# Optimization experiments

Measured on AMD Instinct MI355X. Metric: run time of the kernel, lower is better.

The kernel has to match this reference:

```python
import jax, jax.numpy as jnp
import numpy as np

B, N, D_IN, D_OUT, NHOP = 16, 1024, 128, 128, 3


def setup_inputs() -> dict:
    key = jax.random.key(0)
    ks = jax.random.split(key, 7)
    x = jax.random.normal(ks[0], (B, N, D_IN), dtype=jnp.float32)
    # sparse-ish binary adjacency (float, as in the torch model) with self loops
    adj = (jax.random.uniform(ks[1], (B, N, N)) < 0.05).astype(jnp.float32)
    adj = jnp.maximum(adj, jnp.eye(N, dtype=jnp.float32)[None])
    # learned params (torch nn.Linear default-ish init scale)
    s_in = 1.0 / np.sqrt(D_IN)
    s_out = 1.0 / np.sqrt(2 * D_OUT)
    W_w = jax.random.uniform(ks[2], (D_OUT, D_IN), minval=-s_in, maxval=s_in, dtype=jnp.float32)
    W_b = jax.random.uniform(ks[3], (D_OUT,), minval=-s_in, maxval=s_in, dtype=jnp.float32)
    A = jax.random.normal(ks[4], (D_OUT, D_OUT), dtype=jnp.float32) * 0.02  # nn.Parameter(zeros) would kill signal; use small init
    gate_w = jax.random.uniform(ks[5], (1, 2 * D_OUT), minval=-s_out, maxval=s_out, dtype=jnp.float32)
    gate_b = jax.random.uniform(ks[6], (1,), minval=-s_out, maxval=s_out, dtype=jnp.float32)
    return {"x": x, "adj": adj, "W_w": W_w, "W_b": W_b, "A": A,
            "gate_w": gate_w, "gate_b": gate_b}


def reference(x, adj, W_w, W_b, A, gate_w, gate_b):
    # h = W(x): [B,N,D_OUT]
    h = jnp.einsum('bnd,od->bno', x, W_w) + W_b
    # bilinear score e[b,j,k] = (h A)_j . h_k, symmetrized
    e = jnp.einsum('bjl,bkl->bjk', jnp.einsum('bjd,de->bje', h, A), h)
    e = e + jnp.swapaxes(e, 1, 2)
    # masked softmax over dim=1 (as in the torch code), then re-mask
    att = jnp.where(adj > 0, e, jnp.zeros((), dtype=e.dtype))
    att = jax.nn.softmax(att, axis=1)
    att = att * adj
    retval = h
    for _ in range(NHOP):
        az = jax.nn.relu(jnp.einsum('bij,bjk->bik', att, retval))
        gate_in = jnp.concatenate([h, az], axis=-1)            # [B,N,2*D_OUT]
        coeff = jax.nn.sigmoid(jnp.einsum('bnf,of->bno', gate_in, gate_w) + gate_b)  # [B,N,1]
        retval = coeff * h + (1.0 - coeff) * az
    return retval
```

## Files before the change

### kernel.cpp

```cpp
#include <hip/hip_runtime.h>
#include <math.h>

#define Bn 16
#define Nn 1024
#define Dn 128

typedef unsigned short ushort;
typedef unsigned long long u64;
typedef short short8 __attribute__((ext_vector_type(8)));
typedef float f32x4 __attribute__((ext_vector_type(4)));
typedef ushort us8 __attribute__((ext_vector_type(8)));
typedef ushort us4 __attribute__((ext_vector_type(4)));

__device__ __forceinline__ ushort f2bf(float f) {
    unsigned u = __float_as_uint(f);
    u += 0x7fff + ((u >> 16) & 1);
    return (ushort)(u >> 16);
}
__device__ __forceinline__ float bf2f(ushort s) {
    return __uint_as_float(((unsigned)s) << 16);
}

#if defined(__has_builtin)
#if __has_builtin(__builtin_amdgcn_global_load_lds)
#define HAVE_GLL 1
#endif
#endif
#ifndef HAVE_GLL
#define HAVE_GLL 0
#endif

typedef __attribute__((address_space(1))) void as1_t;
typedef __attribute__((address_space(3))) void as3_t;

__device__ __forceinline__ void stage_group(const void* gbase, void* lbase, int lane) {
#if HAVE_GLL
    __builtin_amdgcn_global_load_lds((as1_t*)((const char*)gbase + lane * 16),
                                     (as3_t*)lbase, 16, 0, 0);
#else
    *(us8*)((char*)lbase + lane * 16) = *(const us8*)((const char*)gbase + lane * 16);
#endif
}


__global__ __launch_bounds__(256) void k_ph0(const float* __restrict__ Ww,
                                             const float* __restrict__ A,
                                             const float* __restrict__ adj,
                                             ushort* __restrict__ Whi, ushort* __restrict__ Wlo,
                                             ushort* __restrict__ Shi, ushort* __restrict__ Slo,
                                             float* __restrict__ Z, u64* __restrict__ bm) {
    int L = blockIdx.x, t = threadIdx.x;
    if (L < 64) {
        int i = L * 256 + t;
        float w = Ww[i];
        ushort wh = f2bf(w);
        Whi[i] = wh;
        Wlo[i] = f2bf(w - bf2f(wh));
        int e = i >> 7, d = i & 127;
        float s = A[i] + A[d * Dn + e];
        ushort sh = f2bf(s);
        Shi[i] = sh;
        Slo[i] = f2bf(s - bf2f(sh));
        Z[i] = (float)Nn;
    }
    int gwv = L * 4 + (t >> 6);
    int lane = t & 63;
    #pragma unroll 4
    for (int it = 0; it < 16; ++it) {
        int pair = gwv * 16 + it;
        const float* p = adj + (size_t)pair * 256 + lane * 4;
        float4 v = *(const float4*)p;
        u64 b0 = __ballot(v.x > 0.f);
        u64 b1 = __ballot(v.y > 0.f);
        u64 b2 = __ballot(v.z > 0.f);
        u64 b3 = __ballot(v.w > 0.f);
        if (lane == 0) {
            u64* d = bm + (size_t)pair * 4;
            d[0] = b0; d[1] = b1; d[2] = b2; d[3] = b3;
        }
    }
}

__global__ __launch_bounds__(256) void k_h(const float* __restrict__ x,
                                           const float* __restrict__ Wb,
                                           const ushort* __restrict__ Whi,
                                           const ushort* __restrict__ Wlo,
                                           const ushort* __restrict__ Shi,
                                           const ushort* __restrict__ Slo,
                                           float* __restrict__ h,
                                           ushort* __restrict__ h16f,
                                           ushort* __restrict__ g16f) {
    int I0 = blockIdx.x * 16;
    int t = threadIdx.x, w = t >> 6, lane = t & 63;
    int m = lane & 15, q = lane >> 4;

    __shared__ float xs[16][Dn + 4];
    __shared__ float hs[16][Dn + 4];
    __shared__ float gs_[16][Dn + 4];

    {
        int r = t >> 4, c8 = (t & 15) * 8;
        const float* src = x + (size_t)(I0 + r) * Dn + c8;
        *(float4*)&xs[r][c8]     = *(const float4*)(src);
        *(float4*)&xs[r][c8 + 4] = *(const float4*)(src + 4);
    }
    __syncthreads();

    f32x4 acc0 = {0,0,0,0}, acc1 = {0,0,0,0};
    #pragma unroll
    for (int ks = 0; ks < 4; ++ks) {
        int k0 = q * 8 + ks * 32;
        float v[8]; short8 ahi, alo;
        *(float4*)(v)     = *(const float4*)(&xs[m][k0]);
        *(float4*)(v + 4) = *(const float4*)(&xs[m][k0 + 4]);
        #pragma unroll
        for (int j = 0; j < 8; ++j) {
            ushort hi = f2bf(v[j]);
            ahi[j] = (short)hi;
            alo[j] = (short)f2bf(v[j] - bf2f(hi));
        }
        #pragma unroll
        for (int nn = 0; nn < 2; ++nn) {
            int brow = (w * 2 + nn) * 16 + m;
            short8 bhi = __builtin_bit_cast(short8, ((const us8*)(Whi + (size_t)brow * Dn))[q + ks * 4]);
            short8 blo = __builtin_bit_cast(short8, ((const us8*)(Wlo + (size_t)brow * Dn))[q + ks * 4]);
            f32x4 acc = nn ? acc1 : acc0;
            acc = __builtin_amdgcn_mfma_f32_16x16x32_bf16(ahi, bhi, acc, 0, 0, 0);
            acc = __builtin_amdgcn_mfma_f32_16x16x32_bf16(alo, bhi, acc, 0, 0, 0);
            acc = __builtin_amdgcn_mfma_f32_16x16x32_bf16(ahi, blo, acc, 0, 0, 0);
            if (nn) acc1 = acc; else acc0 = acc;
        }
    }
    #pragma unroll
    for (int nn = 0; nn < 2; ++nn) {
        int col = (w * 2 + nn) * 16 + m;
        float bias = Wb[col];
        f32x4 acc = nn ? acc1 : acc0;
        #pragma unroll
        for (int r = 0; r < 4; ++r) {
            int rl = q * 4 + r;
            float hv = acc[r] + bias;
            h[(size_t)(I0 + rl) * Dn + col] = hv;
            hs[rl][col] = hv;
        }
    }
    __syncthreads();

    f32x4 bcc0 = {0,0,0,0}, bcc1 = {0,0,0,0};
    #pragma unroll
    for (int ks = 0; ks < 4; ++ks) {
        int k0 = q * 8 + ks * 32;
        float v[8]; short8 ahi, alo;
        *(float4*)(v)     = *(const float4*)(&hs[m][k0]);
        *(float4*)(v + 4) = *(const float4*)(&hs[m][k0 + 4]);
        #pragma unroll
        for (int j = 0; j < 8; ++j) {
            ushort hi = f2bf(v[j]);
            ahi[j] = (short)hi;
            alo[j] = (short)f2bf(v[j] - bf2f(hi));
        }
        #pragma unroll
        for (int nn = 0; nn < 2; ++nn) {
            int brow = (w * 2 + nn) * 16 + m;
            short8 bhi = __builtin_bit_cast(short8, ((const us8*)(Shi + (size_t)brow * Dn))[q + ks * 4]);
            short8 blo = __builtin_bit_cast(short8, ((const us8*)(Slo + (size_t)brow * Dn))[q + ks * 4]);
            f32x4 acc = nn ? bcc1 : bcc0;
            acc = __builtin_amdgcn_mfma_f32_16x16x32_bf16(ahi, bhi, acc, 0, 0, 0);
            acc = __builtin_amdgcn_mfma_f32_16x16x32_bf16(alo, bhi, acc, 0, 0, 0);
            acc = __builtin_amdgcn_mfma_f32_16x16x32_bf16(ahi, blo, acc, 0, 0, 0);
            if (nn) bcc1 = acc; else bcc0 = acc;
        }
    }
    #pragma unroll
    for (int nn = 0; nn < 2; ++nn) {
        int col = (w * 2 + nn) * 16 + m;
        f32x4 acc = nn ? bcc1 : bcc0;
        #pragma unroll
        for (int r = 0; r < 4; ++r)
            gs_[q * 4 + r][col] = acc[r];
    }
    __syncthreads();

    {
        int kc = t >> 6, mm = (t >> 2) & 15, qq = t & 3;
        int cb = kc * 32 + qq * 8;
        us8 oh, oa;
        #pragma unroll
        for (int e = 0; e < 8; ++e) {
            oh[e] = f2bf(hs[mm][cb + e]);
            oa[e] = f2bf(gs_[mm][cb + e]);
        }
        size_t U = (size_t)(I0 >> 4) * 256 + kc * 64 + qq * 16 + mm;
        ((us8*)h16f)[U] = oh;
        ((us8*)g16f)[U] = oa;
    }
}

__global__ __launch_bounds__(256, 4) void k_scores(const ushort* __restrict__ g16f,
                                                   const ushort* __restrict__ h16f,
                                                   const u64* __restrict__ bm,
                                                   ushort* __restrict__ Ef,
                                                   float* __restrict__ Z) {
    int L = blockIdx.x;
    int b    = ((L & 7) << 1) | (L >> 11);
    int tile = (L >> 3) & 255;
    int I0 = (tile >> 4) << 6;
    int J0 = (tile & 15) << 6;
    int t = threadIdx.x, wid = t >> 6, lane = t & 63;
    int loff = lane * 16;

    __shared__ __align__(16) char smem[18432];
    float (*sc)[68] = (float(*)[68])smem;
    float (*cz)[64] = (float(*)[64])(smem + 17408);

    {
        const char* hbp = (const char*)h16f + (size_t)b * 262144;
        for (int g = wid; g < 16; g += 4) {
            int rt_l = g >> 2, kk = g & 3;
            stage_group(hbp + ((size_t)((J0 >> 4) + rt_l) * 256 + kk * 64) * 16,
                        smem + g * 1024, lane);
        }
    }
    short8 afr[4];
    {
        const char* gbp = (const char*)g16f + (size_t)b * 262144
                        + (size_t)((I0 >> 4) + wid) * 4096 + loff;
        #pragma unroll
        for (int ks = 0; ks < 4; ++ks)
            afr[ks] = __builtin_bit_cast(short8, *(const us8*)(gbp + ks * 1024));
    }
    __syncthreads();

    f32x4 acc[4] = {};
    #pragma unroll
    for (int ks = 0; ks < 4; ++ks) {
        #pragma unroll
        for (int nt = 0; nt < 4; ++nt) {
            short8 bb = __builtin_bit_cast(short8,
                *(const us8*)(smem + (nt * 4 + ks) * 1024 + loff));
            acc[nt] = __builtin_amdgcn_mfma_f32_16x16x32_bf16(afr[ks], bb, acc[nt], 0, 0, 0);
        }
    }
    __syncthreads();

    {
        int m = lane & 15, q = lane >> 4;
        #pragma unroll
        for (int nt = 0; nt < 4; ++nt)
            #pragma unroll
            for (int r = 0; r < 4; ++r)
                sc[wid * 16 + q * 4 + r][nt * 16 + m] = acc[nt][r];
    }
    __syncthreads();

    int row16 = t >> 4, c = t & 15;
    int bitc = ((J0 >> 2) & 63) + c;
    float colsum[4] = {0.f, 0.f, 0.f, 0.f};
    #pragma unroll
    for (int it = 0; it < 4; ++it) {
        int row = it * 16 + row16;
        const u64* wp = bm + ((size_t)(b * Nn + I0 + row) * 4 + (J0 >> 8)) * 4;
        u64 wj[4] = {wp[0], wp[1], wp[2], wp[3]};
        float s4[4];
        *(float4*)s4 = *(const float4*)(&sc[row][c * 4]);
        us4 e4;
        #pragma unroll
        for (int j = 0; j < 4; ++j) {
            float ex = __expf(s4[j]);
            bool on = (wj[j] >> bitc) & 1;
            e4[j] = f2bf(on ? ex : 0.f);
            colsum[j] += on ? (ex - 1.0f) : 0.f;
        }
        size_t base = ((((size_t)b * 64 + (I0 >> 4) + it) * 32 + (J0 >> 5) + (c >> 3)) * 512)
                    + (size_t)((c & 7) >> 1) * 128 + row16 * 8 + (c & 1) * 4;
        *(us4*)(Ef + base) = e4;
    }
    #pragma unroll
    for (int j = 0; j < 4; ++j) {
        colsum[j] += __shfl_xor(colsum[j], 16, 64);
        colsum[j] += __shfl_xor(colsum[j], 32, 64);
    }
    if (lane < 16) {
        #pragma unroll
        for (int j = 0; j < 4; ++j) cz[wid][lane * 4 + j] = colsum[j];
    }
    __syncthreads();
    if (t < 64) {
        float s = cz[0][t] + cz[1][t] + cz[2][t] + cz[3][t];
        atomicAdd(&Z[b * Nn + J0 + t], s);
    }
}

__global__ __launch_bounds__(256) void k_prep(const float* __restrict__ src,
                                              const float* __restrict__ Z,
                                              ushort* __restrict__ Tf) {
    int b = blockIdx.y;
    int j0 = blockIdx.x * 64;
    int t = threadIdx.x;
    __shared__ float ls[64][129];
    __shared__ float iz[64];
    if (t < 64) iz[t] = 1.0f / Z[b * Nn + j0 + t];
    __syncthreads();
    #pragma unroll
    for (int it = 0; it < 8; ++it) {
        int idx = it * 256 + t;
        int j = idx >> 5, k4 = (idx & 31) * 4;
        float4 v = *(const float4*)(src + ((size_t)b * Nn + j0 + j) * Dn + k4);
        float z = iz[j];
        ls[j][k4] = v.x * z; ls[j][k4 + 1] = v.y * z;
        ls[j][k4 + 2] = v.z * z; ls[j][k4 + 3] = v.w * z;
    }
    __syncthreads();
    int k = t & 127, half = t >> 7;
    us8 o[4];
    #pragma unroll
    for (int qq = 0; qq < 4; ++qq) {
        us8 tmp;
        #pragma unroll
        for (int e = 0; e < 8; ++e)
            tmp[e] = f2bf(ls[half * 32 + qq * 8 + e][k]);
        o[qq] = tmp;
    }
    size_t G = (size_t)(k >> 4) * 32 + (j0 >> 5) + half;
    ushort* dst = Tf + (size_t)b * 131072 + G * 512 + (size_t)(k & 15) * 8;
    #pragma unroll
    for (int qq = 0; qq < 4; ++qq)
        *(us8*)(dst + qq * 128) = o[qq];
}

#define SSTAGE(BUF, gc) do {                                                           \
    _Pragma("unroll")                                                                  \
    for (int j = 0; j < 8; ++j) {                                                      \
        int g = rr * 8 + j;                         \
        stage_group(tfb + ((size_t)(g >> 2) * 32 + (gc) * 4 + (g & 3)) * 1024,         \
                    sbase + (BUF) * 32768 + g * 1024, lane);                           \
    }                                                                                  \
} while (0)

#define ELD(SET, gc) do {                                                              \
    _Pragma("unroll")                                                                  \
    for (int kk = 0; kk < 4; ++kk)                                                     \
        SET[kk] = __builtin_bit_cast(short8,                                           \
            *(const us8*)(ebase + ((gc) * 4 + kk) * 1024));                            \
} while (0)

#define SMFMA(BUF, SET) do {                                                           \
    __builtin_amdgcn_s_setprio(1);                                                     \
    _Pragma("unroll")                                                                  \
    for (int kk = 0; kk < 4; ++kk) {                                                   \
        _Pragma("unroll")                                                              \
        for (int nt = 0; nt < 8; ++nt) {                                               \
            short8 bf = __builtin_bit_cast(short8,                                     \
                *(const us8*)(sbase + (BUF) * 32768 + (nt * 4 + kk) * 1024 + loff));   \
            acc[nt] = __builtin_amdgcn_mfma_f32_16x16x32_bf16(SET[kk], bf, acc[nt], 0, 0, 0); \
        }                                                                              \
    }                                                                                  \
    __builtin_amdgcn_s_setprio(0);                                                     \
} while (0)

#define WAITB(NC) do {                                                                 \
    asm volatile("s_waitcnt vmcnt(" #NC ")" ::: "memory");                             \
    __builtin_amdgcn_s_barrier();                                                      \
} while (0)

__global__ __launch_bounds__(512, 1) void k_hop(const ushort* __restrict__ Ef,
                                                const ushort* __restrict__ Tf,
                                                const float* __restrict__ h,
                                                const float* __restrict__ Z,
                                                const float* __restrict__ gw,
                                                const float* __restrict__ gb,
                                                ushort* __restrict__ Tfn,
                                                float* __restrict__ out,
                                                int last) {
    int L = blockIdx.x;
    int b   = ((L & 7) << 1) | (L >> 7);
    int rtp = (L >> 3) & 15;
    int t = threadIdx.x, w = t >> 6, lane = t & 63;
    int m = lane & 15, q = lane >> 4;
    int rr = w & 3, ks = w >> 2;
    int rt = rtp * 4 + rr;
    int I0 = rt << 4;
    int loff = lane * 16;

    __shared__ __align__(16) char smem[131072];
    char* sbase = smem + ks * 65536;

    const char* tfb   = (const char*)Tf + (size_t)b * 262144;
    const char* ebase = (const char*)Ef + (size_t)(b * 64 + rt) * 32768 + loff;

    float hv[8][4], izr[4], gwa[8], gwz[8];
    float gb0 = gb[0];
    size_t hbase = ((size_t)b * Nn + I0) * Dn;
    if (ks == 0) {
        #pragma unroll
        for (int r = 0; r < 4; ++r) izr[r] = 1.0f / Z[b * Nn + I0 + q * 4 + r];
        #pragma unroll
        for (int nt = 0; nt < 8; ++nt) {
            gwa[nt] = gw[nt * 16 + m];
            gwz[nt] = gw[Dn + nt * 16 + m];
            #pragma unroll
            for (int r = 0; r < 4; ++r)
                hv[nt][r] = h[hbase + (size_t)(q * 4 + r) * Dn + nt * 16 + m];
        }
    }
    asm volatile("s_waitcnt vmcnt(0)" ::: "memory");

    int gc0 = ks * 4;
    f32x4 acc[8] = {};
    short8 eA[4], eB[4];

    SSTAGE(0, gc0);     ELD(eA, gc0);
    WAITB(4);
    SSTAGE(1, gc0 + 1); ELD(eB, gc0 + 1); SMFMA(0, eA);
    WAITB(4);
    SSTAGE(0, gc0 + 2); ELD(eA, gc0 + 2); SMFMA(1, eB);
    WAITB(4);
    SSTAGE(1, gc0 + 3); ELD(eB, gc0 + 3); SMFMA(0, eA);
    WAITB(4);
                                          SMFMA(1, eB);
    __syncthreads();

    float (*cmb)[8][16][16] = (float(*)[8][16][16])(smem + 65536);
    if (ks == 1) {
        #pragma unroll
        for (int nt = 0; nt < 8; ++nt)
            #pragma unroll
            for (int r = 0; r < 4; ++r)
                cmb[rr][nt][q * 4 + r][m] = acc[nt][r];
    }
    __syncthreads();

    ushort (*tt)[128][16] = (ushort(*)[128][16])smem;
    if (ks == 0) {
        #pragma unroll
        for (int nt = 0; nt < 8; ++nt)
            #pragma unroll
            for (int r = 0; r < 4; ++r)
                acc[nt][r] += cmb[rr][nt][q * 4 + r][m];

        float coef[4];
        #pragma unroll
        for (int r = 0; r < 4; ++r) {
            float gs = 0.f;
            #pragma unroll
            for (int nt = 0; nt < 8; ++nt) {
                float az = fmaxf(acc[nt][r], 0.f);
                acc[nt][r] = az;
                gs += hv[nt][r] * gwa[nt] + az * gwz[nt];
            }
            gs += __shfl_xor(gs, 1, 64);
            gs += __shfl_xor(gs, 2, 64);
            gs += __shfl_xor(gs, 4, 64);
            gs += __shfl_xor(gs, 8, 64);
            coef[r] = 1.0f / (1.0f + __expf(-(gs + gb0)));
        }

        if (last) {
            #pragma unroll
            for (int r = 0; r < 4; ++r) {
                float cc = coef[r];
                #pragma unroll
                for (int nt = 0; nt < 8; ++nt)
                    out[hbase + (size_t)(q * 4 + r) * Dn + nt * 16 + m] =
                        cc * hv[nt][r] + (1.f - cc) * acc[nt][r];
            }
        } else {
            #pragma unroll
            for (int r = 0; r < 4; ++r) {
                float cc = coef[r];
                float iz = izr[r];
                #pragma unroll
                for (int nt = 0; nt < 8; ++nt) {
                    float v = cc * hv[nt][r] + (1.f - cc) * acc[nt][r];
                    tt[rr][nt * 16 + m][q * 4 + r] = f2bf(v * iz);
                }
            }
        }
    }
    if (!last) {
        __syncthreads();
        if (t < 256) {
            int k = t >> 1, jh = t & 1;
            size_t G = (size_t)(k >> 4) * 32 + rtp * 2 + jh;
            ushort* dst = Tfn + (size_t)b * 131072 + G * 512 + (size_t)(k & 15) * 8;
            #pragma unroll
            for (int qq = 0; qq < 4; ++qq)
                *(us8*)(dst + qq * 128) = *(const us8*)&tt[jh * 2 + (qq >> 1)][k][(qq & 1) * 8];
        }
    }
}

extern "C" void kernel_launch(void* const* d_in, const int* in_sizes, int n_in,
                              void* d_out, int out_size, void* d_ws, size_t ws_size,
                              hipStream_t stream) {
    const float* x    = (const float*)d_in[0];
    const float* adj  = (const float*)d_in[1];
    const float* Ww   = (const float*)d_in[2];
    const float* Wb   = (const float*)d_in[3];
    const float* A    = (const float*)d_in[4];
    const float* gw   = (const float*)d_in[5];
    const float* gb   = (const float*)d_in[6];
    float* out = (float*)d_out;

    char* ws = (char*)d_ws;
    float*  h    = (float*)(ws);
    ushort* Ta   = (ushort*)(ws + (8u << 20));
    ushort* Tb   = (ushort*)(ws + (12u << 20));
    ushort* E    = (ushort*)(ws + (16u << 20));
    float*  Z    = (float*)(ws + (48u << 20));
    ushort* Whi  = (ushort*)(ws + (48u << 20) + (64u << 10));
    ushort* Wlo  = (ushort*)(ws + (48u << 20) + (96u << 10));
    ushort* Shi  = (ushort*)(ws + (48u << 20) + (128u << 10));
    ushort* Slo  = (ushort*)(ws + (48u << 20) + (160u << 10));
    u64*    bm   = (u64*)(ws + (48u << 20) + (192u << 10));

    k_ph0   <<<1024, 256, 0, stream>>>(Ww, A, adj, Whi, Wlo, Shi, Slo, Z, bm);
    k_h     <<<1024, 256, 0, stream>>>(x, Wb, Whi, Wlo, Shi, Slo, h, Ta, Tb);
    k_scores<<<4096, 256, 0, stream>>>(Tb, Ta, bm, E, Z);
    k_prep  <<<dim3(16, Bn), 256, 0, stream>>>(h, Z, Ta);
    k_hop   <<<256, 512, 0, stream>>>(E, Ta, h, Z, gw, gb, Tb, out, 0);
    k_hop   <<<256, 512, 0, stream>>>(E, Tb, h, Z, gw, gb, Ta, out, 0);
    k_hop   <<<256, 512, 0, stream>>>(E, Ta, h, Z, gw, gb, (ushort*)nullptr, out, 1);
}
```

Measured before the change: 191.6 us.

## Exploit symmetric score matrix: compute upper-triangle tiles and emit both halves

The symmetrized score matrix is computed only for upper-triangular 64x64 tile pairs (136 per batch instead of 256). Each off-diagonal block writes its tile and the transpose into shared memory, then produces masked exp values and column sums for both (I,J) and (J,I). This roughly halves the MFMA work and the h-tile staging. The price is twice the shared memory per block, which may lower occupancy, plus a serial loop to decode the tile index and more epilogue work per block.

```diff
diff --git a/kernel.cpp b/kernel.cpp
--- a/kernel.cpp
+++ b/kernel.cpp
@@ -202,16 +202,22 @@
                                                    ushort* __restrict__ Ef,
                                                    float* __restrict__ Z) {
     int L = blockIdx.x;
-    int b    = ((L & 7) << 1) | (L >> 11);
-    int tile = (L >> 3) & 255;
-    int I0 = (tile >> 4) << 6;
-    int J0 = (tile & 15) << 6;
+    int rest = L >> 3;
+    int b = (L & 7) * 2 + (rest >= 136);
+    int p = rest - (rest >= 136 ? 136 : 0);
+    int ti = 0;
+    while (p >= 16 - ti) { p -= 16 - ti; ++ti; }
+    int tj = ti + p;
+    int I0 = ti << 6, J0 = tj << 6;
+    int diag = (ti == tj);
     int t = threadIdx.x, wid = t >> 6, lane = t & 63;
     int loff = lane * 16;
 
-    __shared__ __align__(16) char smem[18432];
-    float (*sc)[68] = (float(*)[68])smem;
-    float (*cz)[64] = (float(*)[64])(smem + 17408);
+    __shared__ __align__(16) char smem[36864];
+    float (*sc)[68]  = (float(*)[68])smem;
+    float (*scT)[68] = (float(*)[68])(smem + 17408);
+    float (*czA)[64] = (float(*)[64])(smem + 34816);
+    float (*czB)[64] = (float(*)[64])(smem + 35840);
 
     {
         const char* hbp = (const char*)h16f + (size_t)b * 262144;
@@ -248,46 +254,86 @@
         #pragma unroll
         for (int nt = 0; nt < 4; ++nt)
             #pragma unroll
-            for (int r = 0; r < 4; ++r)
+            for (int r = 0; r < 4; ++r) {
                 sc[wid * 16 + q * 4 + r][nt * 16 + m] = acc[nt][r];
+                if (!diag) scT[nt * 16 + m][wid * 16 + q * 4 + r] = acc[nt][r];
+            }
     }
     __syncthreads();
 
     int row16 = t >> 4, c = t & 15;
-    int bitc = ((J0 >> 2) & 63) + c;
-    float colsum[4] = {0.f, 0.f, 0.f, 0.f};
-    #pragma unroll
-    for (int it = 0; it < 4; ++it) {
-        int row = it * 16 + row16;
-        const u64* wp = bm + ((size_t)(b * Nn + I0 + row) * 4 + (J0 >> 8)) * 4;
-        u64 wj[4] = {wp[0], wp[1], wp[2], wp[3]};
-        float s4[4];
-        *(float4*)s4 = *(const float4*)(&sc[row][c * 4]);
-        us4 e4;
+    {
+        int bitc = ((J0 >> 2) & 63) + c;
+        float colsum[4] = {0.f, 0.f, 0.f, 0.f};
+        #pragma unroll
+        for (int it = 0; it < 4; ++it) {
+            int row = it * 16 + row16;
+            const u64* wp = bm + ((size_t)(b * Nn + I0 + row) * 4 + (J0 >> 8)) * 4;
+            u64 wj[4] = {wp[0], wp[1], wp[2], wp[3]};
+            float s4[4];
+            *(float4*)s4 = *(const float4*)(&sc[row][c * 4]);
+            us4 e4;
+            #pragma unroll
+            for (int j = 0; j < 4; ++j) {
+                float ex = __expf(s4[j]);
+                bool on = (wj[j] >> bitc) & 1;
+                e4[j] = f2bf(on ? ex : 0.f);
+                colsum[j] += on ? (ex - 1.0f) : 0.f;
+            }
+            size_t base = ((((size_t)b * 64 + (I0 >> 4) + it) * 32 + (J0 >> 5) + (c >> 3)) * 512)
+                        + (size_t)((c & 7) >> 1) * 128 + row16 * 8 + (c & 1) * 4;
+            *(us4*)(Ef + base) = e4;
+        }
         #pragma unroll
         for (int j = 0; j < 4; ++j) {
-            float ex = __expf(s4[j]);
-            bool on = (wj[j] >> bitc) & 1;
-            e4[j] = f2bf(on ? ex : 0.f);
-            colsum[j] += on ? (ex - 1.0f) : 0.f;
-        }
-        size_t base = ((((size_t)b * 64 + (I0 >> 4) + it) * 32 + (J0 >> 5) + (c >> 3)) * 512)
-                    + (size_t)((c & 7) >> 1) * 128 + row16 * 8 + (c & 1) * 4;
-        *(us4*)(Ef + base) = e4;
-    }
-    #pragma unroll
-    for (int j = 0; j < 4; ++j) {
-        colsum[j] += __shfl_xor(colsum[j], 16, 64);
-        colsum[j] += __shfl_xor(colsum[j], 32, 64);
-    }
-    if (lane < 16) {
-        #pragma unroll
-        for (int j = 0; j < 4; ++j) cz[wid][lane * 4 + j] = colsum[j];
+            colsum[j] += __shfl_xor(colsum[j], 16, 64);
+            colsum[j] += __shfl_xor(colsum[j], 32, 64);
+        }
+        if (lane < 16) {
+            #pragma unroll
+            for (int j = 0; j < 4; ++j) czA[wid][lane * 4 + j] = colsum[j];
+        }
+    }
+    if (!diag) {
+        int bitc = ((I0 >> 2) & 63) + c;
+        float colsum[4] = {0.f, 0.f, 0.f, 0.f};
+        #pragma unroll
+        for (int it = 0; it < 4; ++it) {
+            int row = it * 16 + row16;
+            const u64* wp = bm + ((size_t)(b * Nn + J0 + row) * 4 + (I0 >> 8)) * 4;
+            u64 wj[4] = {wp[0], wp[1], wp[2], wp[3]};
+            float s4[4];
+            *(float4*)s4 = *(const float4*)(&scT[row][c * 4]);
+            us4 e4;
+            #pragma unroll
+            for (int j = 0; j < 4; ++j) {
+                float ex = __expf(s4[j]);
+                bool on = (wj[j] >> bitc) & 1;
+                e4[j] = f2bf(on ? ex : 0.f);
+                colsum[j] += on ? (ex - 1.0f) : 0.f;
+            }
+            size_t base = ((((size_t)b * 64 + (J0 >> 4) + it) * 32 + (I0 >> 5) + (c >> 3)) * 512)
+                        + (size_t)((c & 7) >> 1) * 128 + row16 * 8 + (c & 1) * 4;
+            *(us4*)(Ef + base) = e4;
+        }
+        #pragma unroll
+        for (int j = 0; j < 4; ++j) {
+            colsum[j] += __shfl_xor(colsum[j], 16, 64);
+            colsum[j] += __shfl_xor(colsum[j], 32, 64);
+        }
+        if (lane < 16) {
+            #pragma unroll
+            for (int j = 0; j < 4; ++j) czB[wid][lane * 4 + j] = colsum[j];
+        }
     }
     __syncthreads();
     if (t < 64) {
-        float s = cz[0][t] + cz[1][t] + cz[2][t] + cz[3][t];
+        float s = czA[0][t] + czA[1][t] + czA[2][t] + czA[3][t];
         atomicAdd(&Z[b * Nn + J0 + t], s);
+        if (!diag) {
+            float s2 = czB[0][t] + czB[1][t] + czB[2][t] + czB[3][t];
+            atomicAdd(&Z[b * Nn + I0 + t], s2);
+        }
     }
 }
 
@@ -516,7 +562,7 @@
 
     k_ph0   <<<1024, 256, 0, stream>>>(Ww, A, adj, Whi, Wlo, Shi, Slo, Z, bm);
     k_h     <<<1024, 256, 0, stream>>>(x, Wb, Whi, Wlo, Shi, Slo, h, Ta, Tb);
-    k_scores<<<4096, 256, 0, stream>>>(Tb, Ta, bm, E, Z);
+    k_scores<<<2176, 256, 0, stream>>>(Tb, Ta, bm, E, Z);
     k_prep  <<<dim3(16, Bn), 256, 0, stream>>>(h, Z, Ta);
     k_hop   <<<256, 512, 0, stream>>>(E, Ta, h, Z, gw, gb, Tb, out, 0);
     k_hop   <<<256, 512, 0, stream>>>(E, Tb, h, Z, gw, gb, Ta, out, 0);
```

Result: no change. 191.9 us (+0.1%).
